# Kernel tuning notes

Measured on AMD Instinct MI355X. Metric: run time of the kernel, lower is better.

The kernel has to match this reference:

```python
import jax, jax.numpy as jnp
import numpy as np

B = 262144
EDGES_SRC = np.array([0, 0, 0, 0])
EDGES_DST = np.array([1, 2, 3, 4])
PRED_IDS = np.array([[0, 10, 14], [1, 11, 18], [2, 12, 22], [3, 13, 26]])
O_IDS = np.array([0, 1, 2, 3, 10, 11, 12, 13, 14, 18, 22, 26])


def _xavier(k, shape):
    fan_out, fan_in = shape
    bound = float(np.sqrt(6.0 / (fan_in + fan_out)))
    return jax.random.uniform(k, shape, jnp.float32, -bound, bound)


def setup_inputs() -> dict:
    key = jax.random.key(0)
    ks = jax.random.split(key, 12)
    return {
        "initial_c": jax.random.uniform(ks[0], (B, 30), jnp.float32),
        "initial_s": jax.random.normal(ks[1], (B, 9), jnp.float32),
        "current_c": jax.random.uniform(ks[2], (B, 30), jnp.float32),
        "eps": jax.random.normal(ks[3], (B, 8), jnp.float32),
        # GnnMessagePassing params (torch Linear: y = x @ W.T + b)
        "W1": _xavier(ks[4], (128, 13)), "b1": jnp.zeros(128, jnp.float32),
        "W2": _xavier(ks[5], (39, 128)), "b2": jnp.zeros(39, jnp.float32),
        "W3": _xavier(ks[6], (128, 39)), "b3": jnp.zeros(128, jnp.float32),
        "Wm": _xavier(ks[7], (8, 128)), "bm": jnp.zeros(8, jnp.float32),
        "Wv": _xavier(ks[8], (8, 128)), "bv": jnp.zeros(8, jnp.float32),
        # Decoder params: [25 -> 32 -> 12], sigmoid output (binary=True)
        "Wd1": _xavier(ks[9], (32, 25)), "bd1": jnp.zeros(32, jnp.float32),
        "Wd2": _xavier(ks[10], (12, 32)), "bd2": jnp.zeros(12, jnp.float32),
    }


def reference(initial_c, initial_s, current_c, eps,
              W1, b1, W2, b2, W3, b3, Wm, bm, Wv, bv, Wd1, bd1, Wd2, bd2):
    bsz = current_c.shape[0]
    eye = jnp.eye(5, dtype=current_c.dtype)
    # per-edge constant one-hot pair features: [4, 10]
    edge_onehot = jnp.concatenate([eye[EDGES_SRC], eye[EDGES_DST]], axis=-1)
    edge_onehot = jnp.broadcast_to(edge_onehot[:, None, :], (4, bsz, 10))
    # gather predicate triplets per edge: [B, 4, 3] -> [4, B, 3]
    preds = jnp.transpose(current_c[:, PRED_IDS], (1, 0, 2))
    inp_mp = jnp.concatenate([edge_onehot, preds], axis=-1)  # [4, B, 13]

    # message MLP + sum over edge dim
    x = jax.nn.relu(jnp.einsum('ebi,oi->ebo', inp_mp, W1) + b1)  # [4, B, 128]
    x = jax.nn.relu(jnp.einsum('ebi,oi->ebo', x, W2) + b2)       # [4, B, 39]
    x = x.sum(axis=0)                                            # [B, 39]
    x = jax.nn.relu(x @ W3.T + b3)                               # [B, 128]
    means = x @ Wm.T + bm                                        # [B, 8]
    log_var = x @ Wv.T + bv                                      # [B, 8]

    # reparameterization
    z = eps * jnp.exp(0.5 * log_var) + means

    # decoder: [one-hot(node 0) | initial_c[o_ids] | z] -> sigmoid MLP
    node0 = jnp.broadcast_to(eye[0], (bsz, 5))
    inp_dec = jnp.concatenate([node0, initial_c[:, O_IDS], z], axis=1)  # [B, 25]
    h = jax.nn.relu(inp_dec @ Wd1.T + bd1)
    recon_x = jax.nn.sigmoid(h @ Wd2.T + bd2)  # [B, 12]
    return recon_x, means, log_var, z
```

## Files before the change

### kernel.cpp

```cpp
#include <hip/hip_runtime.h>
#include <hip/hip_bf16.h>

#define TPB 256
#define PREP_BLOCKS 64

typedef __attribute__((ext_vector_type(8))) short short8;
typedef __attribute__((ext_vector_type(4))) float f32x4;

#define G_W2F   0
#define G_MVF   12288
#define G_D1F   16384
#define G_D2F   18432
#define G_CEAB  19456
#define G_B2P   23552
#define G_B3    23744
#define G_BMV   24256
#define G_D1C   24320
#define G_BD2   24448
#define G_W3F   24512
#define G_END   40896

__device__ __forceinline__ unsigned short f2bf(float f) {
    unsigned int u = __float_as_uint(f);
    unsigned int r = u + 0x7fffu + ((u >> 16) & 1u);
    return (unsigned short)(r >> 16);
}
__device__ __forceinline__ unsigned int pk(float a, float b) {
    __hip_bfloat162 h = __float22bfloat162_rn(make_float2(a, b));
    unsigned int u; __builtin_memcpy(&u, &h, 4); return u;
}
__device__ __forceinline__ unsigned short bfbits(float v) {
    return (unsigned short)(pk(v, v) & 0xffffu);
}

__global__ void prep_kernel(
    const float* __restrict__ W1, const float* __restrict__ b1,
    const float* __restrict__ W2, const float* __restrict__ b2,
    const float* __restrict__ W3, const float* __restrict__ b3,
    const float* __restrict__ Wm, const float* __restrict__ bm,
    const float* __restrict__ Wv, const float* __restrict__ bv,
    const float* __restrict__ Wd1, const float* __restrict__ bd1,
    const float* __restrict__ Wd2, const float* __restrict__ bd2,
    unsigned char* __restrict__ ws)
{
    const int g0 = blockIdx.x * TPB + threadIdx.x;
    const int gs = gridDim.x * TPB;
    unsigned short* w2f = (unsigned short*)(ws + G_W2F);
    for (int i = g0; i < 6144; i += gs) {
        int j = i & 7, lane = (i >> 3) & 63, ts = i >> 9;
        int t = ts >> 2, s = ts & 3, q = lane >> 4;
        int n = 16 * t + (lane & 15);
        int phys = 16 * (2 * s + (j >> 2)) + 4 * q + (j & 3);
        w2f[i] = (n < 39) ? f2bf(W2[n * 128 + phys]) : 0;
    }
    unsigned short* w3f = (unsigned short*)(ws + G_W3F);
    for (int i = g0; i < 8192; i += gs) {
        int j = i & 7, lane = (i >> 3) & 63, ns = i >> 9;
        int nt = ns >> 1, s = ns & 1, q = lane >> 4;
        int n = 16 * nt + (lane & 15);
        int phys = 16 * (2 * s + (j >> 2)) + 4 * q + (j & 3);
        w3f[i] = (phys < 39) ? f2bf(W3[n * 39 + phys]) : 0;
    }
    unsigned short* mvf = (unsigned short*)(ws + G_MVF);
    for (int i = g0; i < 2048; i += gs) {
        int j = i & 7, lane = (i >> 3) & 63, s = i >> 9;
        int q = lane >> 4, n = lane & 15;
        int phys = 16 * (2 * s + (j >> 2)) + 4 * q + (j & 3);
        mvf[i] = f2bf(n < 8 ? Wm[n * 128 + phys] : Wv[(n - 8) * 128 + phys]);
    }
    unsigned short* d1f = (unsigned short*)(ws + G_D1F);
    for (int i = g0; i < 1024; i += gs) {
        int j = i & 7, lane = (i >> 3) & 63, tt = i >> 9;
        int q = lane >> 4, n = 16 * tt + (lane & 15);
        float v = 0.f;
        if (q == 0)      v = Wd1[n * 25 + 5 + j];
        else if (j < 4)  v = Wd1[n * 25 + 13 + 4 * (q - 1) + j];
        d1f[i] = (q == 0 || j < 4) ? f2bf(v) : 0;
    }
    unsigned short* d2f = (unsigned short*)(ws + G_D2F);
    for (int i = g0; i < 512; i += gs) {
        int j = i & 7, lane = i >> 3;
        int q = lane >> 4, n = lane & 15;
        int phys = 16 * (j >> 2) + 4 * q + (j & 3);
        d2f[i] = (n < 12) ? f2bf(Wd2[n * 32 + phys]) : 0;
    }
    unsigned short* ceab = (unsigned short*)(ws + G_CEAB);
    for (int i = g0; i < 2048; i += gs) {
        int mt = i & 7, lane = (i >> 3) & 63, e = i >> 9;
        int q = lane >> 4, n = 16 * mt + (lane & 15);
        float v = (q == 0) ? W1[n * 13 + 10]
                : (q == 1) ? W1[n * 13 + 11]
                : (q == 2) ? W1[n * 13 + 12]
                           : (W1[n * 13 + 0] + W1[n * 13 + 6 + e] + b1[n]);
        ceab[i] = f2bf(v);
    }
    float* fb = (float*)(ws + G_B2P);
    for (int i = g0; i < 48; i += gs) fb[i] = (i < 39) ? b2[i] : 0.f;
    fb = (float*)(ws + G_B3);
    for (int i = g0; i < 128; i += gs) fb[i] = b3[i];
    fb = (float*)(ws + G_BMV);
    for (int i = g0; i < 16; i += gs) fb[i] = (i < 8) ? bm[i] : bv[i - 8];
    fb = (float*)(ws + G_D1C);
    for (int i = g0; i < 32; i += gs) fb[i] = Wd1[i * 25 + 0] + bd1[i];
    fb = (float*)(ws + G_BD2);
    for (int i = g0; i < 16; i += gs) fb[i] = (i < 12) ? bd2[i] : 0.f;
}

union S8 { short8 v; uint4 u; };

#define MFMA(a, b, c) __builtin_amdgcn_mfma_f32_16x16x32_bf16(a, b, c, 0, 0, 0)

__global__ __launch_bounds__(TPB, 2) void vae_mfma(
    const float* __restrict__ ic, const float* __restrict__ cc,
    const float* __restrict__ eps,
    const unsigned char* __restrict__ ws,
    float* __restrict__ out, int B)
{
    __shared__ __attribute__((aligned(16))) unsigned char lds[G_END];
    const int tid = threadIdx.x;

    {
        const uint4* src = (const uint4*)ws;
        uint4* dst = (uint4*)lds;
        #pragma unroll
        for (int it = 0; it < 10; it++) {
            int idx = it * TPB + tid;
            if (idx < G_END / 16) dst[idx] = src[idx];
        }
    }
    __syncthreads();

    const int lane = tid & 63, w = tid >> 6;
    const int quad = lane >> 4, n16 = lane & 15;
    const long rb = ((long)blockIdx.x * 4 + w) * 16;
    const long Rl = rb + n16;

    unsigned int bpv[4];
    {
        const float* crow = cc + Rl * 30;
        float pv0, pv1, pv2, pv3;
        if (quad == 0) {
            float2 t0 = *(const float2*)(crow);
            float2 t1 = *(const float2*)(crow + 2);
            pv0 = t0.x; pv1 = t0.y; pv2 = t1.x; pv3 = t1.y;
        } else if (quad == 1) {
            float2 t0 = *(const float2*)(crow + 10);
            float2 t1 = *(const float2*)(crow + 12);
            pv0 = t0.x; pv1 = t0.y; pv2 = t1.x; pv3 = t1.y;
        } else if (quad == 2) {
            pv0 = crow[14]; pv1 = crow[18]; pv2 = crow[22]; pv3 = crow[26];
        } else {
            pv0 = pv1 = pv2 = pv3 = 1.0f;
        }
        bpv[0] = (unsigned int)bfbits(pv0);
        bpv[1] = (unsigned int)bfbits(pv1);
        bpv[2] = (unsigned int)bfbits(pv2);
        bpv[3] = (unsigned int)bfbits(pv3);
    }

    S8 W2F[12];
    #pragma unroll
    for (int ts = 0; ts < 12; ts++)
        W2F[ts].u = *(const uint4*)(lds + G_W2F + (ts * 64 + lane) * 16);
    const float* b2p = (const float*)(lds + G_B2P);
    f32x4 b2q[3];
    #pragma unroll
    for (int t = 0; t < 3; t++)
        b2q[t] = *(const f32x4*)(b2p + 16 * t + 4 * quad);

    f32x4 ss0 = {0,0,0,0}, ss1 = {0,0,0,0}, ss2 = {0,0,0,0};

    #pragma unroll
    for (int e = 0; e < 4; e++) {
        S8 bp;
        bp.u.x = bpv[e]; bp.u.y = 0u; bp.u.z = 0u; bp.u.w = 0u;
        S8 ce8;
        ce8.u = *(const uint4*)(lds + G_CEAB + e * 1024 + lane * 16);
        S8 xf[4];
        #pragma unroll
        for (int mt = 0; mt < 8; mt++) {
            unsigned int cws[4] = {ce8.u.x, ce8.u.y, ce8.u.z, ce8.u.w};
            unsigned int cw = cws[mt >> 1];
            S8 af;
            af.u.x = (mt & 1) ? (cw >> 16) : (cw & 0xffffu);
            af.u.y = 0u; af.u.z = 0u; af.u.w = 0u;
            f32x4 z4 = {0,0,0,0};
            f32x4 cr = MFMA(af.v, bp.v, z4);
            unsigned int lo = pk(fmaxf(cr[0], 0.f), fmaxf(cr[1], 0.f));
            unsigned int hi = pk(fmaxf(cr[2], 0.f), fmaxf(cr[3], 0.f));
            if ((mt & 1) == 0) { xf[mt >> 1].u.x = lo; xf[mt >> 1].u.y = hi; }
            else               { xf[mt >> 1].u.z = lo; xf[mt >> 1].u.w = hi; }
        }
        f32x4 c0 = b2q[0], c1 = b2q[1], c2 = b2q[2];
        #pragma unroll
        for (int s = 0; s < 4; s++) {
            c0 = MFMA(W2F[s].v,     xf[s].v, c0);
            c1 = MFMA(W2F[4 + s].v, xf[s].v, c1);
            c2 = MFMA(W2F[8 + s].v, xf[s].v, c2);
        }
        #pragma unroll
        for (int r = 0; r < 4; r++) {
            ss0[r] += fmaxf(c0[r], 0.f);
            ss1[r] += fmaxf(c1[r], 0.f);
            ss2[r] += fmaxf(c2[r], 0.f);
        }
    }

    S8 sf0, sf1;
    sf0.u.x = pk(ss0[0], ss0[1]); sf0.u.y = pk(ss0[2], ss0[3]);
    sf0.u.z = pk(ss1[0], ss1[1]); sf0.u.w = pk(ss1[2], ss1[3]);
    sf1.u.x = pk(ss2[0], ss2[1]); sf1.u.y = pk(ss2[2], ss2[3]);
    sf1.u.z = 0u; sf1.u.w = 0u;

    const uint4* w3l = (const uint4*)(lds + G_W3F);
    const float* b3p = (const float*)(lds + G_B3);
    S8 hf[4];
    #pragma unroll
    for (int nt = 0; nt < 8; nt++) {
        f32x4 c = *(const f32x4*)(b3p + nt * 16 + 4 * quad);
        S8 a0, a1;
        a0.u = w3l[(nt * 2 + 0) * 64 + lane];
        a1.u = w3l[(nt * 2 + 1) * 64 + lane];
        c = MFMA(a0.v, sf0.v, c);
        c = MFMA(a1.v, sf1.v, c);
        unsigned int lo = pk(fmaxf(c[0], 0.f), fmaxf(c[1], 0.f));
        unsigned int hi = pk(fmaxf(c[2], 0.f), fmaxf(c[3], 0.f));
        if ((nt & 1) == 0) { hf[nt >> 1].u.x = lo; hf[nt >> 1].u.y = hi; }
        else               { hf[nt >> 1].u.z = lo; hf[nt >> 1].u.w = hi; }
    }

    f32x4 cm  = *(const f32x4*)((const float*)(lds + G_BMV) + 4 * quad);
    f32x4 cm2 = *(const f32x4*)((const float*)(lds + G_BMV) + 4 * ((quad + 2) & 3));
    const int laneSw = quad * 16 + ((n16 + 8) & 15);
    #pragma unroll
    for (int s = 0; s < 4; s++) {
        S8 a, a2;
        a.u  = *(const uint4*)(lds + G_MVF + (s * 64 + lane) * 16);
        a2.u = *(const uint4*)(lds + G_MVF + (s * 64 + laneSw) * 16);
        cm  = MFMA(a.v,  hf[s].v, cm);
        cm2 = MFMA(a2.v, hf[s].v, cm2);
    }

    float4 ev = *(const float4*)(eps + Rl * 8 + 4 * (quad & 1));
    f32x4 zz;
    {
        const bool lo2 = (quad < 2);
        float mn0 = lo2 ? cm[0] : cm2[0], lv0 = lo2 ? cm2[0] : cm[0];
        float mn1 = lo2 ? cm[1] : cm2[1], lv1 = lo2 ? cm2[1] : cm[1];
        float mn2 = lo2 ? cm[2] : cm2[2], lv2 = lo2 ? cm2[2] : cm[2];
        float mn3 = lo2 ? cm[3] : cm2[3], lv3 = lo2 ? cm2[3] : cm[3];
        zz[0] = fmaf(ev.x, __expf(0.5f * lv0), mn0);
        zz[1] = fmaf(ev.y, __expf(0.5f * lv1), mn1);
        zz[2] = fmaf(ev.z, __expf(0.5f * lv2), mn2);
        zz[3] = fmaf(ev.w, __expf(0.5f * lv3), mn3);
    }
    float* pml = (float*)((quad < 2) ? (out + (long)B * 12) : (out + (long)B * 20));
    *(float4*)(pml + Rl * 8 + 4 * (quad & 1)) = *(float4*)&cm;
    if (quad < 2)
        *(float4*)(out + (long)B * 28 + Rl * 8 + 4 * quad) = *(float4*)&zz;

    S8 df;
    if (quad == 0) {
        const float* irow = ic + Rl * 30;
        float2 a0 = *(const float2*)(irow);
        float2 a1 = *(const float2*)(irow + 2);
        float2 a2 = *(const float2*)(irow + 10);
        float2 a3 = *(const float2*)(irow + 12);
        df.u.x = pk(a0.x, a0.y); df.u.y = pk(a1.x, a1.y);
        df.u.z = pk(a2.x, a2.y); df.u.w = pk(a3.x, a3.y);
    } else if (quad == 1) {
        const float* irow = ic + Rl * 30;
        df.u.x = pk(irow[14], irow[18]);
        df.u.y = pk(irow[22], irow[26]);
        df.u.z = 0u; df.u.w = 0u;
    } else {
        df.u.x = pk(zz[0], zz[1]);
        df.u.y = pk(zz[2], zz[3]);
        df.u.z = 0u; df.u.w = 0u;
    }

    const float* d1c = (const float*)(lds + G_D1C);
    S8 a;
    f32x4 ct = *(const f32x4*)(d1c + 4 * quad);
    a.u = *(const uint4*)(lds + G_D1F + (0 * 64 + lane) * 16);
    f32x4 h0 = MFMA(a.v, df.v, ct);
    ct = *(const f32x4*)(d1c + 16 + 4 * quad);
    a.u = *(const uint4*)(lds + G_D1F + (1 * 64 + lane) * 16);
    f32x4 h1 = MFMA(a.v, df.v, ct);
    S8 hf2;
    hf2.u.x = pk(fmaxf(h0[0], 0.f), fmaxf(h0[1], 0.f));
    hf2.u.y = pk(fmaxf(h0[2], 0.f), fmaxf(h0[3], 0.f));
    hf2.u.z = pk(fmaxf(h1[0], 0.f), fmaxf(h1[1], 0.f));
    hf2.u.w = pk(fmaxf(h1[2], 0.f), fmaxf(h1[3], 0.f));

    f32x4 c2 = *(const f32x4*)((const float*)(lds + G_BD2) + 4 * quad);
    S8 a2; a2.u = *(const uint4*)(lds + G_D2F + lane * 16);
    c2 = MFMA(a2.v, hf2.v, c2);
    if (quad < 3) {
        float4 o;
        o.x = 1.f / (1.f + __expf(-c2[0]));
        o.y = 1.f / (1.f + __expf(-c2[1]));
        o.z = 1.f / (1.f + __expf(-c2[2]));
        o.w = 1.f / (1.f + __expf(-c2[3]));
        *(float4*)(out + Rl * 12 + 4 * quad) = o;
    }
}

extern "C" void kernel_launch(void* const* d_in, const int* in_sizes, int n_in,
                              void* d_out, int out_size, void* d_ws, size_t ws_size,
                              hipStream_t stream) {
    const float* ic  = (const float*)d_in[0];
    const float* cc  = (const float*)d_in[2];
    const float* eps = (const float*)d_in[3];

    const int B = in_sizes[3] / 8;
    const int nblocks = B / 64;

    prep_kernel<<<PREP_BLOCKS, TPB, 0, stream>>>(
        (const float*)d_in[4],  (const float*)d_in[5],
        (const float*)d_in[6],  (const float*)d_in[7],
        (const float*)d_in[8],  (const float*)d_in[9],
        (const float*)d_in[10], (const float*)d_in[11],
        (const float*)d_in[12], (const float*)d_in[13],
        (const float*)d_in[14], (const float*)d_in[15],
        (const float*)d_in[16], (const float*)d_in[17],
        (unsigned char*)d_ws);
    vae_mfma<<<nblocks, TPB, 0, stream>>>(
        ic, cc, eps, (const unsigned char*)d_ws, (float*)d_out, B);
}
```

Baseline: 177.9 us.

## Process two 16-row tiles per wave to reuse LDS weight fragments

Each wave now handles 32 rows as two independent 16-row tiles (A and B), so every weight fragment read from LDS feeds two MFMAs, and the grid is halved. W2 fragments are no longer kept resident in registers across the edge loop but are reloaded per step and shared by both tiles. The aim is to cut LDS weight traffic and the per-block weight-staging cost per row, and to give the scheduler two independent MFMA chains to interleave. The cost is higher register pressure and fewer blocks, which may lower occupancy or cause spills.

```diff
diff --git a/kernel.cpp b/kernel.cpp
--- a/kernel.cpp
+++ b/kernel.cpp
@@ -132,12 +132,13 @@
 
     const int lane = tid & 63, w = tid >> 6;
     const int quad = lane >> 4, n16 = lane & 15;
-    const long rb = ((long)blockIdx.x * 4 + w) * 16;
-    const long Rl = rb + n16;
-
-    unsigned int bpv[4];
-    {
-        const float* crow = cc + Rl * 30;
+    const long rb = ((long)blockIdx.x * 4 + w) * 32;
+    const long RlA = rb + n16, RlB = rb + 16 + n16;
+
+    unsigned int bpvA[4], bpvB[4];
+    #pragma unroll
+    for (int t = 0; t < 2; t++) {
+        const float* crow = cc + (t ? RlB : RlA) * 30;
         float pv0, pv1, pv2, pv3;
         if (quad == 0) {
             float2 t0 = *(const float2*)(crow);
@@ -152,31 +153,25 @@
         } else {
             pv0 = pv1 = pv2 = pv3 = 1.0f;
         }
-        bpv[0] = (unsigned int)bfbits(pv0);
-        bpv[1] = (unsigned int)bfbits(pv1);
-        bpv[2] = (unsigned int)bfbits(pv2);
-        bpv[3] = (unsigned int)bfbits(pv3);
-    }
-
-    S8 W2F[12];
-    #pragma unroll
-    for (int ts = 0; ts < 12; ts++)
-        W2F[ts].u = *(const uint4*)(lds + G_W2F + (ts * 64 + lane) * 16);
+        unsigned int* dst = t ? bpvB : bpvA;
+        dst[0] = (unsigned int)bfbits(pv0);
+        dst[1] = (unsigned int)bfbits(pv1);
+        dst[2] = (unsigned int)bfbits(pv2);
+        dst[3] = (unsigned int)bfbits(pv3);
+    }
+
     const float* b2p = (const float*)(lds + G_B2P);
-    f32x4 b2q[3];
-    #pragma unroll
-    for (int t = 0; t < 3; t++)
-        b2q[t] = *(const f32x4*)(b2p + 16 * t + 4 * quad);
-
-    f32x4 ss0 = {0,0,0,0}, ss1 = {0,0,0,0}, ss2 = {0,0,0,0};
+    f32x4 ssA0 = {0,0,0,0}, ssA1 = {0,0,0,0}, ssA2 = {0,0,0,0};
+    f32x4 ssB0 = {0,0,0,0}, ssB1 = {0,0,0,0}, ssB2 = {0,0,0,0};
 
     #pragma unroll
     for (int e = 0; e < 4; e++) {
-        S8 bp;
-        bp.u.x = bpv[e]; bp.u.y = 0u; bp.u.z = 0u; bp.u.w = 0u;
+        S8 bpA, bpB;
+        bpA.u.x = bpvA[e]; bpA.u.y = 0u; bpA.u.z = 0u; bpA.u.w = 0u;
+        bpB.u.x = bpvB[e]; bpB.u.y = 0u; bpB.u.z = 0u; bpB.u.w = 0u;
         S8 ce8;
         ce8.u = *(const uint4*)(lds + G_CEAB + e * 1024 + lane * 16);
-        S8 xf[4];
+        S8 xfA[4], xfB[4];
         #pragma unroll
         for (int mt = 0; mt < 8; mt++) {
             unsigned int cws[4] = {ce8.u.x, ce8.u.y, ce8.u.z, ce8.u.w};
@@ -185,124 +180,172 @@
             af.u.x = (mt & 1) ? (cw >> 16) : (cw & 0xffffu);
             af.u.y = 0u; af.u.z = 0u; af.u.w = 0u;
             f32x4 z4 = {0,0,0,0};
-            f32x4 cr = MFMA(af.v, bp.v, z4);
-            unsigned int lo = pk(fmaxf(cr[0], 0.f), fmaxf(cr[1], 0.f));
-            unsigned int hi = pk(fmaxf(cr[2], 0.f), fmaxf(cr[3], 0.f));
-            if ((mt & 1) == 0) { xf[mt >> 1].u.x = lo; xf[mt >> 1].u.y = hi; }
-            else               { xf[mt >> 1].u.z = lo; xf[mt >> 1].u.w = hi; }
-        }
-        f32x4 c0 = b2q[0], c1 = b2q[1], c2 = b2q[2];
+            f32x4 crA = MFMA(af.v, bpA.v, z4);
+            f32x4 crB = MFMA(af.v, bpB.v, z4);
+            unsigned int loA = pk(fmaxf(crA[0], 0.f), fmaxf(crA[1], 0.f));
+            unsigned int hiA = pk(fmaxf(crA[2], 0.f), fmaxf(crA[3], 0.f));
+            unsigned int loB = pk(fmaxf(crB[0], 0.f), fmaxf(crB[1], 0.f));
+            unsigned int hiB = pk(fmaxf(crB[2], 0.f), fmaxf(crB[3], 0.f));
+            if ((mt & 1) == 0) {
+                xfA[mt >> 1].u.x = loA; xfA[mt >> 1].u.y = hiA;
+                xfB[mt >> 1].u.x = loB; xfB[mt >> 1].u.y = hiB;
+            } else {
+                xfA[mt >> 1].u.z = loA; xfA[mt >> 1].u.w = hiA;
+                xfB[mt >> 1].u.z = loB; xfB[mt >> 1].u.w = hiB;
+            }
+        }
+        f32x4 cA0 = *(const f32x4*)(b2p + 4 * quad);
+        f32x4 cA1 = *(const f32x4*)(b2p + 16 + 4 * quad);
+        f32x4 cA2 = *(const f32x4*)(b2p + 32 + 4 * quad);
+        f32x4 cB0 = cA0, cB1 = cA1, cB2 = cA2;
         #pragma unroll
         for (int s = 0; s < 4; s++) {
-            c0 = MFMA(W2F[s].v,     xf[s].v, c0);
-            c1 = MFMA(W2F[4 + s].v, xf[s].v, c1);
-            c2 = MFMA(W2F[8 + s].v, xf[s].v, c2);
+            S8 w0, w1, w2;
+            w0.u = *(const uint4*)(lds + G_W2F + ((s) * 64 + lane) * 16);
+            w1.u = *(const uint4*)(lds + G_W2F + ((4 + s) * 64 + lane) * 16);
+            w2.u = *(const uint4*)(lds + G_W2F + ((8 + s) * 64 + lane) * 16);
+            cA0 = MFMA(w0.v, xfA[s].v, cA0);
+            cB0 = MFMA(w0.v, xfB[s].v, cB0);
+            cA1 = MFMA(w1.v, xfA[s].v, cA1);
+            cB1 = MFMA(w1.v, xfB[s].v, cB1);
+            cA2 = MFMA(w2.v, xfA[s].v, cA2);
+            cB2 = MFMA(w2.v, xfB[s].v, cB2);
         }
         #pragma unroll
         for (int r = 0; r < 4; r++) {
-            ss0[r] += fmaxf(c0[r], 0.f);
-            ss1[r] += fmaxf(c1[r], 0.f);
-            ss2[r] += fmaxf(c2[r], 0.f);
-        }
-    }
-
-    S8 sf0, sf1;
-    sf0.u.x = pk(ss0[0], ss0[1]); sf0.u.y = pk(ss0[2], ss0[3]);
-    sf0.u.z = pk(ss1[0], ss1[1]); sf0.u.w = pk(ss1[2], ss1[3]);
-    sf1.u.x = pk(ss2[0], ss2[1]); sf1.u.y = pk(ss2[2], ss2[3]);
-    sf1.u.z = 0u; sf1.u.w = 0u;
+            ssA0[r] += fmaxf(cA0[r], 0.f);
+            ssA1[r] += fmaxf(cA1[r], 0.f);
+            ssA2[r] += fmaxf(cA2[r], 0.f);
+            ssB0[r] += fmaxf(cB0[r], 0.f);
+            ssB1[r] += fmaxf(cB1[r], 0.f);
+            ssB2[r] += fmaxf(cB2[r], 0.f);
+        }
+    }
+
+    S8 sfA0, sfA1, sfB0, sfB1;
+    sfA0.u.x = pk(ssA0[0], ssA0[1]); sfA0.u.y = pk(ssA0[2], ssA0[3]);
+    sfA0.u.z = pk(ssA1[0], ssA1[1]); sfA0.u.w = pk(ssA1[2], ssA1[3]);
+    sfA1.u.x = pk(ssA2[0], ssA2[1]); sfA1.u.y = pk(ssA2[2], ssA2[3]);
+    sfA1.u.z = 0u; sfA1.u.w = 0u;
+    sfB0.u.x = pk(ssB0[0], ssB0[1]); sfB0.u.y = pk(ssB0[2], ssB0[3]);
+    sfB0.u.z = pk(ssB1[0], ssB1[1]); sfB0.u.w = pk(ssB1[2], ssB1[3]);
+    sfB1.u.x = pk(ssB2[0], ssB2[1]); sfB1.u.y = pk(ssB2[2], ssB2[3]);
+    sfB1.u.z = 0u; sfB1.u.w = 0u;
 
     const uint4* w3l = (const uint4*)(lds + G_W3F);
     const float* b3p = (const float*)(lds + G_B3);
-    S8 hf[4];
+    S8 hfA[4], hfB[4];
     #pragma unroll
     for (int nt = 0; nt < 8; nt++) {
-        f32x4 c = *(const f32x4*)(b3p + nt * 16 + 4 * quad);
+        f32x4 cb3 = *(const f32x4*)(b3p + nt * 16 + 4 * quad);
         S8 a0, a1;
         a0.u = w3l[(nt * 2 + 0) * 64 + lane];
         a1.u = w3l[(nt * 2 + 1) * 64 + lane];
-        c = MFMA(a0.v, sf0.v, c);
-        c = MFMA(a1.v, sf1.v, c);
-        unsigned int lo = pk(fmaxf(c[0], 0.f), fmaxf(c[1], 0.f));
-        unsigned int hi = pk(fmaxf(c[2], 0.f), fmaxf(c[3], 0.f));
-        if ((nt & 1) == 0) { hf[nt >> 1].u.x = lo; hf[nt >> 1].u.y = hi; }
-        else               { hf[nt >> 1].u.z = lo; hf[nt >> 1].u.w = hi; }
-    }
-
-    f32x4 cm  = *(const f32x4*)((const float*)(lds + G_BMV) + 4 * quad);
-    f32x4 cm2 = *(const f32x4*)((const float*)(lds + G_BMV) + 4 * ((quad + 2) & 3));
+        f32x4 cA = cb3, cB = cb3;
+        cA = MFMA(a0.v, sfA0.v, cA);
+        cB = MFMA(a0.v, sfB0.v, cB);
+        cA = MFMA(a1.v, sfA1.v, cA);
+        cB = MFMA(a1.v, sfB1.v, cB);
+        unsigned int loA = pk(fmaxf(cA[0], 0.f), fmaxf(cA[1], 0.f));
+        unsigned int hiA = pk(fmaxf(cA[2], 0.f), fmaxf(cA[3], 0.f));
+        unsigned int loB = pk(fmaxf(cB[0], 0.f), fmaxf(cB[1], 0.f));
+        unsigned int hiB = pk(fmaxf(cB[2], 0.f), fmaxf(cB[3], 0.f));
+        if ((nt & 1) == 0) {
+            hfA[nt >> 1].u.x = loA; hfA[nt >> 1].u.y = hiA;
+            hfB[nt >> 1].u.x = loB; hfB[nt >> 1].u.y = hiB;
+        } else {
+            hfA[nt >> 1].u.z = loA; hfA[nt >> 1].u.w = hiA;
+            hfB[nt >> 1].u.z = loB; hfB[nt >> 1].u.w = hiB;
+        }
+    }
+
+    f32x4 cmb  = *(const f32x4*)((const float*)(lds + G_BMV) + 4 * quad);
+    f32x4 cmb2 = *(const f32x4*)((const float*)(lds + G_BMV) + 4 * ((quad + 2) & 3));
+    f32x4 cmA = cmb, cm2A = cmb2, cmB = cmb, cm2B = cmb2;
     const int laneSw = quad * 16 + ((n16 + 8) & 15);
     #pragma unroll
     for (int s = 0; s < 4; s++) {
         S8 a, a2;
         a.u  = *(const uint4*)(lds + G_MVF + (s * 64 + lane) * 16);
         a2.u = *(const uint4*)(lds + G_MVF + (s * 64 + laneSw) * 16);
-        cm  = MFMA(a.v,  hf[s].v, cm);
-        cm2 = MFMA(a2.v, hf[s].v, cm2);
-    }
-
-    float4 ev = *(const float4*)(eps + Rl * 8 + 4 * (quad & 1));
-    f32x4 zz;
-    {
-        const bool lo2 = (quad < 2);
-        float mn0 = lo2 ? cm[0] : cm2[0], lv0 = lo2 ? cm2[0] : cm[0];
-        float mn1 = lo2 ? cm[1] : cm2[1], lv1 = lo2 ? cm2[1] : cm[1];
-        float mn2 = lo2 ? cm[2] : cm2[2], lv2 = lo2 ? cm2[2] : cm[2];
-        float mn3 = lo2 ? cm[3] : cm2[3], lv3 = lo2 ? cm2[3] : cm[3];
-        zz[0] = fmaf(ev.x, __expf(0.5f * lv0), mn0);
-        zz[1] = fmaf(ev.y, __expf(0.5f * lv1), mn1);
-        zz[2] = fmaf(ev.z, __expf(0.5f * lv2), mn2);
-        zz[3] = fmaf(ev.w, __expf(0.5f * lv3), mn3);
-    }
-    float* pml = (float*)((quad < 2) ? (out + (long)B * 12) : (out + (long)B * 20));
-    *(float4*)(pml + Rl * 8 + 4 * (quad & 1)) = *(float4*)&cm;
-    if (quad < 2)
-        *(float4*)(out + (long)B * 28 + Rl * 8 + 4 * quad) = *(float4*)&zz;
-
-    S8 df;
-    if (quad == 0) {
-        const float* irow = ic + Rl * 30;
-        float2 a0 = *(const float2*)(irow);
-        float2 a1 = *(const float2*)(irow + 2);
-        float2 a2 = *(const float2*)(irow + 10);
-        float2 a3 = *(const float2*)(irow + 12);
-        df.u.x = pk(a0.x, a0.y); df.u.y = pk(a1.x, a1.y);
-        df.u.z = pk(a2.x, a2.y); df.u.w = pk(a3.x, a3.y);
-    } else if (quad == 1) {
-        const float* irow = ic + Rl * 30;
-        df.u.x = pk(irow[14], irow[18]);
-        df.u.y = pk(irow[22], irow[26]);
-        df.u.z = 0u; df.u.w = 0u;
-    } else {
-        df.u.x = pk(zz[0], zz[1]);
-        df.u.y = pk(zz[2], zz[3]);
-        df.u.z = 0u; df.u.w = 0u;
+        cmA  = MFMA(a.v,  hfA[s].v, cmA);
+        cmB  = MFMA(a.v,  hfB[s].v, cmB);
+        cm2A = MFMA(a2.v, hfA[s].v, cm2A);
+        cm2B = MFMA(a2.v, hfB[s].v, cm2B);
     }
 
     const float* d1c = (const float*)(lds + G_D1C);
-    S8 a;
-    f32x4 ct = *(const f32x4*)(d1c + 4 * quad);
-    a.u = *(const uint4*)(lds + G_D1F + (0 * 64 + lane) * 16);
-    f32x4 h0 = MFMA(a.v, df.v, ct);
-    ct = *(const f32x4*)(d1c + 16 + 4 * quad);
-    a.u = *(const uint4*)(lds + G_D1F + (1 * 64 + lane) * 16);
-    f32x4 h1 = MFMA(a.v, df.v, ct);
-    S8 hf2;
-    hf2.u.x = pk(fmaxf(h0[0], 0.f), fmaxf(h0[1], 0.f));
-    hf2.u.y = pk(fmaxf(h0[2], 0.f), fmaxf(h0[3], 0.f));
-    hf2.u.z = pk(fmaxf(h1[0], 0.f), fmaxf(h1[1], 0.f));
-    hf2.u.w = pk(fmaxf(h1[2], 0.f), fmaxf(h1[3], 0.f));
-
-    f32x4 c2 = *(const f32x4*)((const float*)(lds + G_BD2) + 4 * quad);
-    S8 a2; a2.u = *(const uint4*)(lds + G_D2F + lane * 16);
-    c2 = MFMA(a2.v, hf2.v, c2);
-    if (quad < 3) {
-        float4 o;
-        o.x = 1.f / (1.f + __expf(-c2[0]));
-        o.y = 1.f / (1.f + __expf(-c2[1]));
-        o.z = 1.f / (1.f + __expf(-c2[2]));
-        o.w = 1.f / (1.f + __expf(-c2[3]));
-        *(float4*)(out + Rl * 12 + 4 * quad) = o;
+    f32x4 ct0 = *(const f32x4*)(d1c + 4 * quad);
+    f32x4 ct1 = *(const f32x4*)(d1c + 16 + 4 * quad);
+    S8 ad10, ad11, ad2;
+    ad10.u = *(const uint4*)(lds + G_D1F + (0 * 64 + lane) * 16);
+    ad11.u = *(const uint4*)(lds + G_D1F + (1 * 64 + lane) * 16);
+    ad2.u  = *(const uint4*)(lds + G_D2F + lane * 16);
+    f32x4 bd2q = *(const f32x4*)((const float*)(lds + G_BD2) + 4 * quad);
+
+    #pragma unroll
+    for (int t = 0; t < 2; t++) {
+        const long Rl = t ? RlB : RlA;
+        f32x4 cm  = t ? cmB  : cmA;
+        f32x4 cm2 = t ? cm2B : cm2A;
+
+        float4 ev = *(const float4*)(eps + Rl * 8 + 4 * (quad & 1));
+        f32x4 zz;
+        {
+            const bool lo2 = (quad < 2);
+            float mn0 = lo2 ? cm[0] : cm2[0], lv0 = lo2 ? cm2[0] : cm[0];
+            float mn1 = lo2 ? cm[1] : cm2[1], lv1 = lo2 ? cm2[1] : cm[1];
+            float mn2 = lo2 ? cm[2] : cm2[2], lv2 = lo2 ? cm2[2] : cm[2];
+            float mn3 = lo2 ? cm[3] : cm2[3], lv3 = lo2 ? cm2[3] : cm[3];
+            zz[0] = fmaf(ev.x, __expf(0.5f * lv0), mn0);
+            zz[1] = fmaf(ev.y, __expf(0.5f * lv1), mn1);
+            zz[2] = fmaf(ev.z, __expf(0.5f * lv2), mn2);
+            zz[3] = fmaf(ev.w, __expf(0.5f * lv3), mn3);
+        }
+        float* pml = (float*)((quad < 2) ? (out + (long)B * 12)
+                                         : (out + (long)B * 20));
+        *(float4*)(pml + Rl * 8 + 4 * (quad & 1)) = *(float4*)&cm;
+        if (quad < 2)
+            *(float4*)(out + (long)B * 28 + Rl * 8 + 4 * quad) = *(float4*)&zz;
+
+        S8 df;
+        if (quad == 0) {
+            const float* irow = ic + Rl * 30;
+            float2 a0 = *(const float2*)(irow);
+            float2 a1 = *(const float2*)(irow + 2);
+            float2 a2 = *(const float2*)(irow + 10);
+            float2 a3 = *(const float2*)(irow + 12);
+            df.u.x = pk(a0.x, a0.y); df.u.y = pk(a1.x, a1.y);
+            df.u.z = pk(a2.x, a2.y); df.u.w = pk(a3.x, a3.y);
+        } else if (quad == 1) {
+            const float* irow = ic + Rl * 30;
+            df.u.x = pk(irow[14], irow[18]);
+            df.u.y = pk(irow[22], irow[26]);
+            df.u.z = 0u; df.u.w = 0u;
+        } else {
+            df.u.x = pk(zz[0], zz[1]);
+            df.u.y = pk(zz[2], zz[3]);
+            df.u.z = 0u; df.u.w = 0u;
+        }
+
+        f32x4 h0 = MFMA(ad10.v, df.v, ct0);
+        f32x4 h1 = MFMA(ad11.v, df.v, ct1);
+        S8 hf2;
+        hf2.u.x = pk(fmaxf(h0[0], 0.f), fmaxf(h0[1], 0.f));
+        hf2.u.y = pk(fmaxf(h0[2], 0.f), fmaxf(h0[3], 0.f));
+        hf2.u.z = pk(fmaxf(h1[0], 0.f), fmaxf(h1[1], 0.f));
+        hf2.u.w = pk(fmaxf(h1[2], 0.f), fmaxf(h1[3], 0.f));
+
+        f32x4 c2 = bd2q;
+        c2 = MFMA(ad2.v, hf2.v, c2);
+        if (quad < 3) {
+            float4 o;
+            o.x = 1.f / (1.f + __expf(-c2[0]));
+            o.y = 1.f / (1.f + __expf(-c2[1]));
+            o.z = 1.f / (1.f + __expf(-c2[2]));
+            o.w = 1.f / (1.f + __expf(-c2[3]));
+            *(float4*)(out + Rl * 12 + 4 * quad) = o;
+        }
     }
 }
 
@@ -314,7 +357,7 @@
     const float* eps = (const float*)d_in[3];
 
     const int B = in_sizes[3] / 8;
-    const int nblocks = B / 64;
+    const int nblocks = B / 128;
 
     prep_kernel<<<PREP_BLOCKS, TPB, 0, stream>>>(
         (const float*)d_in[4],  (const float*)d_in[5],
```

Measured after the change: 181.9 us. 1.02x slower.
